# Optimization experiments

Hardware: AMD Instinct MI355X
Metric: run time of the kernel (lower is better)

Reference implementation:

```python
import jax, jax.numpy as jnp
import numpy as np

L_SEG = 20   # number of CFT segments (hard-coded in original forward)
M_CHEB = 8   # Chebyshev quadrature order per segment


def _cft_magnitude(x, modes):
    """|CFT(x)| at integer frequencies [0, modes).

    Faithful to vectorized_batched_cft_decomposed with L=20, M=8, but only
    evaluated at the first `modes` frequencies (identical values; the original
    computes all rfft freqs then slices). Segment loop is folded into a single
    einsum by absorbing the per-segment phase shift into the quadrature weights.
    x: (B, C, N) real. Returns (B, C, modes) float.
    """
    n = x.shape[-1]
    t = jnp.linspace(0.0, 1.0, n)
    freqs = jnp.arange(modes, dtype=x.dtype)  # rfftfreq(n, d=1/n)[:modes]
    seg_len = 1.0 / L_SEG
    starts = jnp.linspace(0.0, 1.0, L_SEG + 1)[:-1]  # (L,)
    k = jnp.arange(M_CHEB, dtype=x.dtype)
    cheb = -jnp.cos((2.0 * k + 1.0) * jnp.pi / (2.0 * M_CHEB))  # (M,) nodes in [-1,1]
    T = jnp.cos(k[:, None] * jnp.arccos(cheb)[None, :])  # (K=M, M) Chebyshev T_k at nodes
    angle = cheb[:, None] * (freqs[None, :] * (2.0 * jnp.pi * seg_len / 2.0))  # (M, F)
    Wr = jnp.einsum('km,mf->kf', T, jnp.cos(angle)) * (seg_len / 2.0)  # (M, F)
    Wi = jnp.einsum('km,mf->kf', T, -jnp.sin(angle)) * (seg_len / 2.0)
    # piecewise-linear interpolation of x at the Chebyshev nodes of every segment
    t_seg = starts[:, None] + seg_len / 2.0 * (cheb + 1.0)[None, :]  # (L, M)
    right = jnp.clip(jnp.searchsorted(t, t_seg), 0, n - 1)
    left = jnp.clip(right - 1, 0, None)
    t_l, t_r = t[left], t[right]
    denom = jnp.where(t_r - t_l == 0.0, 1.0, t_r - t_l)
    w_r = (t_seg - t_l) / denom
    w_l = 1.0 - w_r
    seg = w_l * x[:, :, left] + w_r * x[:, :, right]  # (B, C, L, M)
    # per-segment phase shift exp(-i*2*pi*f*a) folded into combined weights
    phi = 2.0 * jnp.pi * starts[:, None] * freqs[None, :]  # (L, F)
    cs, sn = jnp.cos(phi), jnp.sin(phi)
    Ar = Wr[None] * cs[:, None, :] + Wi[None] * sn[:, None, :]   # (L, M, F)
    Ai = -Wr[None] * sn[:, None, :] + Wi[None] * cs[:, None, :]
    real = jnp.einsum('bclm,lmf->bcf', seg, Ar)
    imag = jnp.einsum('bclm,lmf->bcf', seg, Ai)
    return jnp.sqrt(real * real + imag * imag)


def setup_inputs() -> dict:
    key = jax.random.key(0)
    ks = jax.random.split(key, 4)
    B, Cin, Cout, N, modes = 32, 64, 64, 8192, 32
    scale = 1.0 / (Cin * Cout)
    return {
        'x': jax.random.normal(ks[0], (B, Cin, N), dtype=jnp.float32),
        'w1_real': scale * jax.random.uniform(ks[1], (Cin, Cout, modes), dtype=jnp.float32),
        'w1_imag': scale * jax.random.uniform(ks[2], (Cin, Cout, modes), dtype=jnp.float32),
        'gate_w': jax.random.normal(ks[3], (Cout, Cin), dtype=jnp.float32) / np.sqrt(Cin),
        'ln_gamma': jnp.ones((modes,), dtype=jnp.float32),
        'ln_beta': jnp.zeros((modes,), dtype=jnp.float32),
    }


def reference(x, w1_real, w1_imag, gate_w, ln_gamma, ln_beta):
    n = x.shape[-1]
    n_rfft = n // 2 + 1
    modes = w1_real.shape[-1]
    x_fft = jnp.fft.rfft(x)  # (B, C, n_rfft) complex64
    # CFT magnitude is detached in the original (x_cft.detach())
    mag = jax.lax.stop_gradient(_cft_magnitude(x, modes))  # (B, C, modes)
    # LayerNorm over the modes axis (eps = 1e-5, torch default)
    mu = jnp.mean(mag, axis=-1, keepdims=True)
    var = jnp.mean((mag - mu) ** 2, axis=-1, keepdims=True)
    g_norm = (mag - mu) / jnp.sqrt(var + 1e-5) * ln_gamma + ln_beta
    # 1x1 conv (no bias) over channels, then sigmoid gate
    gate = jax.nn.sigmoid(jnp.einsum('oi,bif->bof', gate_w, g_norm))  # (B, Cout, modes)
    gated = x_fft[:, :, :modes] * gate  # requires Cin == Cout
    w1 = w1_real + 1j * w1_imag  # (Cin, Cout, modes) complex
    out_modes = jnp.einsum('bix,iox->box', gated, w1)
    pad = jnp.zeros(out_modes.shape[:2] + (n_rfft - modes,), dtype=out_modes.dtype)
    out_ft = jnp.concatenate([out_modes, pad], axis=-1)
    return jnp.fft.irfft(out_ft, n=n)
```

## Files before the change

### kernel.cpp

```cpp
#include <hip/hip_runtime.h>
#include <hip/hip_bf16.h>
#include <math.h>

#define NN    8192
#define NROWS 2048
#define FF    32
#define LM    160

static constexpr int TRIG   = 0;
static constexpr int W1RT   = 524288;
static constexpr int W1IT   = 655360;
static constexpr int GWT    = 786432;
static constexpr int AR_    = 790528;
static constexpr int AI_    = 795648;
static constexpr int WL_    = 800768;
static constexpr int WR_    = 800928;
static constexpr int IL_    = 801088;
static constexpr int IR_    = 801248;
static constexpr int XR_    = 801408;
static constexpr int XI_    = 866944;
static constexpr int GN_    = 932480;
static constexpr int ARAI   = 998016;
static constexpr int TRIGT_ = 1129088;

#define PI_D 3.14159265358979323846

__device__ __forceinline__ void load_lds16(const float* g, float* l) {
  __builtin_amdgcn_global_load_lds(
      (const __attribute__((address_space(1))) void*)g,
      (__attribute__((address_space(3))) void*)l, 16, 0, 0);
}

__global__ __launch_bounds__(256) void k_trig(float* __restrict__ ws) {
  int idx = blockIdx.x * 256 + threadIdx.x;
  int k4 = idx >> 8, f = (idx >> 2) & 63, j = idx & 3;
  int n = 4 * k4 + j;
  int fr = f & 31;
  int p = (fr * n) & (NN - 1);
  float ang = (float)p * (float)(2.0 * PI_D / (double)NN);
  float s, c;
  sincosf(ang, &s, &c);
  float v = (f < 32) ? c : s;
  ws[TRIG + idx] = v;
  ws[TRIGT_ + f * NN + n] = v;
}

__global__ __launch_bounds__(256) void k_cft_tables(float* __restrict__ ws) {
  int tid = blockIdx.x * 256 + threadIdx.x;
  if (tid >= LM * FF) return;
  int j = tid >> 5, f = tid & 31;
  int l = j >> 3, m = j & 7;
  const double cheb[8] = {
    -0.98078528040323044913, -0.83146961230254523708,
    -0.55557023301960222474, -0.19509032201612826785,
     0.19509032201612826785,  0.55557023301960222474,
     0.83146961230254523708,  0.98078528040323044913 };

  double Wr = 0.0, Wi = 0.0;
  #pragma unroll
  for (int mm = 0; mm < 8; ++mm) {
    double c = cheb[mm];
    double T;
    if (m == 0) T = 1.0;
    else {
      double a = 1.0, b = c;
      for (int q = 1; q < m; ++q) { double t = 2.0 * c * b - a; a = b; b = t; }
      T = b;
    }
    double ang = c * (double)f * (PI_D * 0.05);
    Wr += T * cos(ang);
    Wi += T * (-sin(ang));
  }
  Wr *= 0.025; Wi *= 0.025;
  double phi = 2.0 * PI_D * ((double)l * 0.05) * (double)f;
  double cs = cos(phi), sn = sin(phi);
  ws[AR_ + j * FF + f] = (float)(Wr * cs + Wi * sn);
  ws[AI_ + j * FF + f] = (float)(-Wr * sn + Wi * cs);

  if (f == 0) {
    double v = (double)l * 0.05 + 0.025 * (cheb[m] + 1.0);
    int r = (int)(v * 8191.0);
    while ((double)r / 8191.0 < v) ++r;
    while (r > 0 && (double)(r - 1) / 8191.0 >= v) --r;
    if (r > 8191) r = 8191;
    int le = r - 1; if (le < 0) le = 0;
    double tl = (double)le / 8191.0, tr = (double)r / 8191.0;
    double den = (tr - tl == 0.0) ? 1.0 : (tr - tl);
    double wr = (v - tl) / den;
    ws[WL_ + j] = (float)(1.0 - wr);
    ws[WR_ + j] = (float)wr;
    ((int*)ws)[IL_ + j] = le;
    ((int*)ws)[IR_ + j] = r;
  }
}

__global__ __launch_bounds__(256) void k_transpose(const float* __restrict__ w1r,
                                                   const float* __restrict__ w1i,
                                                   const float* __restrict__ gw,
                                                   float* __restrict__ ws) {
  int idx = blockIdx.x * 256 + threadIdx.x;
  if (idx >= 32 * 64 * 64) return;
  int o = idx & 63, i = (idx >> 6) & 63, f = idx >> 12;
  ws[W1RT + (f * 64 + i) * 64 + o] = w1r[(i * 64 + o) * FF + f];
  ws[W1IT + (f * 64 + i) * 64 + o] = w1i[(i * 64 + o) * FF + f];
  if (idx < 4096) {
    ws[GWT + idx] = gw[(idx & 63) * 64 + (idx >> 6)];
  }
}

__global__ __launch_bounds__(256) void k_fwd_gemm(const float* __restrict__ x,
                                                  const float* __restrict__ ws,
                                                  float* __restrict__ part) {
  __shared__ __align__(16) float xs[64 * 128];
  __shared__ __align__(16) float ts[32 * 256];
  const int rt = blockIdx.x >> 6, kc = blockIdx.x & 63;
  const int t = threadIdx.x;
  const int w = t >> 6, lane = t & 63;
  const int half = lane >> 5, fl = lane & 31;
  const int rblock = rt * 64;
  const int kb = kc * 128;
  const int c4 = t & 31, r0 = t >> 5;

  #pragma unroll
  for (int p = 0; p < 8; ++p) {
    int row = r0 + 8 * p;
    load_lds16(x + (size_t)(rblock + row) * NN + kb + c4 * 4,
               &xs[row * 128 + c4 * 4]);
  }
  const float* __restrict__ tsrc = ws + TRIG + (size_t)kc * 8192;
  #pragma unroll
  for (int p = 0; p < 8; ++p) {
    int q = 256 * p + t;
    load_lds16(tsrc + q * 4, &ts[q * 4]);
  }

  float accC[8], accS[8];
  #pragma unroll
  for (int r = 0; r < 8; ++r) { accC[r] = 0.f; accS[r] = 0.f; }

  __syncthreads();

  const float* __restrict__ xb = &xs[(w * 16 + half * 8) * 128];
  const float* __restrict__ tb = &ts[fl * 4];

  #pragma unroll 8
  for (int it = 0; it < 32; ++it) {
    float4 tc = *(const float4*)(tb + it * 256);
    float4 tn = *(const float4*)(tb + it * 256 + 128);
    #pragma unroll
    for (int j = 0; j < 8; ++j) {
      float4 xv = *(const float4*)(xb + j * 128 + it * 4);
      accC[j] = fmaf(xv.w, tc.w, fmaf(xv.z, tc.z,
                fmaf(xv.y, tc.y, fmaf(xv.x, tc.x, accC[j]))));
      accS[j] = fmaf(xv.w, tn.w, fmaf(xv.z, tn.z,
                fmaf(xv.y, tn.y, fmaf(xv.x, tn.x, accS[j]))));
    }
  }

  float* __restrict__ pp = part + ((size_t)kc * NROWS + rblock + w * 16 + half * 8) * 64;
  #pragma unroll
  for (int j = 0; j < 8; ++j) {
    pp[j * 64 + fl]      = accC[j];
    pp[j * 64 + 32 + fl] = accS[j];
  }
}

__global__ __launch_bounds__(256) void k_fred(const float* __restrict__ part,
                                              float* __restrict__ ws) {
  int idx = blockIdx.x * 256 + threadIdx.x;
  int row = idx >> 4, fq = idx & 15;
  const float4* __restrict__ p4 = (const float4*)part;
  float4 s = make_float4(0.f, 0.f, 0.f, 0.f);
  #pragma unroll 16
  for (int kc = 0; kc < 64; ++kc) {
    float4 v = p4[((size_t)kc * NROWS + row) * 16 + fq];
    s.x += v.x; s.y += v.y; s.z += v.z; s.w += v.w;
  }
  if (fq < 8) {
    *(float4*)(ws + XR_ + row * FF + fq * 4) = s;
  } else {
    float4 n = make_float4(-s.x, -s.y, -s.z, -s.w);
    *(float4*)(ws + XI_ + row * FF + (fq - 8) * 4) = n;
  }
}

__global__ __launch_bounds__(256) void k_cft(const float* __restrict__ x,
                                             const float* __restrict__ gamma,
                                             const float* __restrict__ beta,
                                             float* __restrict__ ws) {
  const int sub = threadIdx.x >> 6, li = threadIdx.x & 63;
  const int row = blockIdx.x * 4 + sub;
  const float* __restrict__ xr = x + (size_t)row * NN;
  __shared__ float seg[4][LM];
  #pragma unroll
  for (int g = 0; g < 3; ++g) {
    int j = li + 64 * g;
    if (j < LM) {
      int il = ((const int*)ws)[IL_ + j];
      int ir = ((const int*)ws)[IR_ + j];
      seg[sub][j] = ws[WL_ + j] * xr[il] + ws[WR_ + j] * xr[ir];
    }
  }
  __syncthreads();
  if (li < FF) {
    float re = 0.f, im = 0.f;
    #pragma unroll 8
    for (int j = 0; j < LM; ++j) {
      float sv = seg[sub][j];
      re = fmaf(sv, ws[AR_ + j * FF + li], re);
      im = fmaf(sv, ws[AI_ + j * FF + li], im);
    }
    float mag = sqrtf(re * re + im * im);
    float mu = mag;
    mu += __shfl_xor(mu, 1);  mu += __shfl_xor(mu, 2);  mu += __shfl_xor(mu, 4);
    mu += __shfl_xor(mu, 8);  mu += __shfl_xor(mu, 16);
    mu *= (1.0f / 32.0f);
    float d = mag - mu;
    float vv = d * d;
    vv += __shfl_xor(vv, 1);  vv += __shfl_xor(vv, 2);  vv += __shfl_xor(vv, 4);
    vv += __shfl_xor(vv, 8);  vv += __shfl_xor(vv, 16);
    vv *= (1.0f / 32.0f);
    float g = d / sqrtf(vv + 1e-5f) * gamma[li] + beta[li];
    ws[GN_ + row * FF + li] = g;
  }
}

__global__ __launch_bounds__(64) void k_gate(float* __restrict__ ws) {
  int bidx = blockIdx.x;
  int b = bidx >> 5, f = bidx & 31;
  int o = threadIdx.x;
  __shared__ float gn[64], gr[64], gi[64];
  int rowb = b * 64;
  gn[o] = ws[GN_ + (rowb + o) * FF + f];
  float xre = ws[XR_ + (rowb + o) * FF + f];
  float xim = ws[XI_ + (rowb + o) * FF + f];
  __syncthreads();
  float acc = 0.f;
  #pragma unroll 16
  for (int i = 0; i < 64; ++i)
    acc = fmaf(ws[GWT + i * 64 + o], gn[i], acc);
  float gate = 1.0f / (1.0f + expf(-acc));
  gr[o] = xre * gate;
  gi[o] = xim * gate;
  __syncthreads();
  float Yr = 0.f, Yi = 0.f;
  const float* __restrict__ w1rt = ws + W1RT + f * 4096;
  const float* __restrict__ w1it = ws + W1IT + f * 4096;
  #pragma unroll 8
  for (int i = 0; i < 64; ++i) {
    float a = gr[i], bb2 = gi[i];
    float wr = w1rt[i * 64 + o], wi = w1it[i * 64 + o];
    Yr = fmaf(a, wr, Yr); Yr = fmaf(-bb2, wi, Yr);
    Yi = fmaf(a, wi, Yi); Yi = fmaf(bb2, wr, Yi);
  }
  float* A = ws + ARAI + (size_t)(rowb + o) * 64;
  if (f == 0) {
    A[0]  = Yr * (1.0f / (float)NN);
    A[32] = 0.0f;
  } else {
    A[f]      = Yr * (2.0f / (float)NN);
    A[32 + f] = -Yi * (2.0f / (float)NN);
  }
}

__global__ __launch_bounds__(256) void k_inv(const float* __restrict__ ws,
                                             float* __restrict__ out) {
  __shared__ __align__(16) float As[32 * 64];
  const int blk = blockIdx.x;
  const int bb = blk >> 5, cc = blk & 31;
  const int t = threadIdx.x;
  const int w = t >> 6, lane = t & 63;
  const int rowbase = bb * 32;
  const float* __restrict__ trigt = ws + TRIGT_;
  const int colb = cc * 256 + lane * 4;

  float4 tg0 = *(const float4*)(trigt + (size_t)0 * NN + colb);
  float4 tg1 = *(const float4*)(trigt + (size_t)1 * NN + colb);
  float4 tg2 = *(const float4*)(trigt + (size_t)2 * NN + colb);
  float4 tg3 = *(const float4*)(trigt + (size_t)3 * NN + colb);

  #pragma unroll
  for (int p = 0; p < 2; ++p) {
    int idx = t + 256 * p;
    int r = idx >> 4, q = idx & 15;
    *(float4*)(&As[r * 64 + q * 4]) =
        *(const float4*)(ws + ARAI + (size_t)(rowbase + r) * 64 + q * 4);
  }

  float4 acc[8];
  #pragma unroll
  for (int r = 0; r < 8; ++r) acc[r] = make_float4(0.f, 0.f, 0.f, 0.f);

  __syncthreads();

#define INV_STEP(F0)                                                            \
  {                                                                             \
    _Pragma("unroll")                                                           \
    for (int r = 0; r < 8; ++r) {                                               \
      float4 av = *(const float4*)(&As[(w * 8 + r) * 64 + (F0)]);               \
      acc[r].x = fmaf(av.x, tg0.x, acc[r].x); acc[r].y = fmaf(av.x, tg0.y, acc[r].y); \
      acc[r].z = fmaf(av.x, tg0.z, acc[r].z); acc[r].w = fmaf(av.x, tg0.w, acc[r].w); \
      acc[r].x = fmaf(av.y, tg1.x, acc[r].x); acc[r].y = fmaf(av.y, tg1.y, acc[r].y); \
      acc[r].z = fmaf(av.y, tg1.z, acc[r].z); acc[r].w = fmaf(av.y, tg1.w, acc[r].w); \
      acc[r].x = fmaf(av.z, tg2.x, acc[r].x); acc[r].y = fmaf(av.z, tg2.y, acc[r].y); \
      acc[r].z = fmaf(av.z, tg2.z, acc[r].z); acc[r].w = fmaf(av.z, tg2.w, acc[r].w); \
      acc[r].x = fmaf(av.w, tg3.x, acc[r].x); acc[r].y = fmaf(av.w, tg3.y, acc[r].y); \
      acc[r].z = fmaf(av.w, tg3.z, acc[r].z); acc[r].w = fmaf(av.w, tg3.w, acc[r].w); \
    }                                                                           \
  }

  for (int fo = 0; fo < 15; ++fo) {
    int f0 = fo * 4;
    float4 n0 = *(const float4*)(trigt + (size_t)(f0 + 4) * NN + colb);
    float4 n1 = *(const float4*)(trigt + (size_t)(f0 + 5) * NN + colb);
    float4 n2 = *(const float4*)(trigt + (size_t)(f0 + 6) * NN + colb);
    float4 n3 = *(const float4*)(trigt + (size_t)(f0 + 7) * NN + colb);
    INV_STEP(f0);
    tg0 = n0; tg1 = n1; tg2 = n2; tg3 = n3;
  }
  INV_STEP(60);
#undef INV_STEP

  #pragma unroll
  for (int r = 0; r < 8; ++r) {
    int row = rowbase + w * 8 + r;
    *(float4*)(out + (size_t)row * NN + colb) = acc[r];
  }
}

extern "C" void kernel_launch(void* const* d_in, const int* in_sizes, int n_in,
                              void* d_out, int out_size, void* d_ws, size_t ws_size,
                              hipStream_t stream) {
  const float* x     = (const float*)d_in[0];
  const float* w1r   = (const float*)d_in[1];
  const float* w1i   = (const float*)d_in[2];
  const float* gw    = (const float*)d_in[3];
  const float* gamma = (const float*)d_in[4];
  const float* beta  = (const float*)d_in[5];
  float* out = (float*)d_out;
  float* ws = (float*)d_ws;
  float* part = (float*)d_out;

  hipLaunchKernelGGL(k_trig,       dim3(2048), dim3(256), 0, stream, ws);
  hipLaunchKernelGGL(k_cft_tables, dim3(20),   dim3(256), 0, stream, ws);
  hipLaunchKernelGGL(k_transpose,  dim3(512),  dim3(256), 0, stream, w1r, w1i, gw, ws);
  hipLaunchKernelGGL(k_fwd_gemm,   dim3(2048), dim3(256), 0, stream, x, ws, part);
  hipLaunchKernelGGL(k_fred,       dim3(128),  dim3(256), 0, stream, part, ws);
  hipLaunchKernelGGL(k_cft,        dim3(512),  dim3(256), 0, stream, x, gamma, beta, ws);
  hipLaunchKernelGGL(k_gate,       dim3(1024), dim3(64),  0, stream, ws);
  hipLaunchKernelGGL(k_inv,        dim3(2048), dim3(256), 0, stream, ws, out);
}
```

Before: 214.9 us.

## Exploit half-period symmetry to halve forward and inverse DFT trig work

The forward DFT now folds x[n] and x[n+N/2] into sum and difference terms, so even frequencies use the sum and odd frequencies use the difference. This halves the trig table and the reduction length per block. The inverse DFT splits accumulation into even- and odd-frequency parts over half the columns, then writes both halves as E+O and E-O. Grid sizes and the trig table size are halved. The cost is extra LDS for the u/v buffers and twice as many accumulator registers in the inverse kernel.

Result: faster. 179.9 us (-16.3%).

```diff
diff --git a/kernel.cpp b/kernel.cpp
--- a/kernel.cpp
+++ b/kernel.cpp
@@ -3,6 +3,7 @@
 #include <math.h>
 
 #define NN    8192
+#define NH    4096
 #define NROWS 2048
 #define FF    32
 #define LM    160
@@ -33,8 +34,8 @@
 
 __global__ __launch_bounds__(256) void k_trig(float* __restrict__ ws) {
   int idx = blockIdx.x * 256 + threadIdx.x;
-  int k4 = idx >> 8, f = (idx >> 2) & 63, j = idx & 3;
-  int n = 4 * k4 + j;
+  int k4 = idx >> 8, f = (idx >> 2) & 63, e = idx & 3;
+  int n = 4 * k4 + e;
   int fr = f & 31;
   int p = (fr * n) & (NN - 1);
   float ang = (float)p * (float)(2.0 * PI_D / (double)NN);
@@ -42,7 +43,7 @@
   sincosf(ang, &s, &c);
   float v = (f < 32) ? c : s;
   ws[TRIG + idx] = v;
-  ws[TRIGT_ + f * NN + n] = v;
+  ws[TRIGT_ + f * NH + n] = v;
 }
 
 __global__ __launch_bounds__(256) void k_cft_tables(float* __restrict__ ws) {
@@ -111,45 +112,51 @@
 __global__ __launch_bounds__(256) void k_fwd_gemm(const float* __restrict__ x,
                                                   const float* __restrict__ ws,
                                                   float* __restrict__ part) {
-  __shared__ __align__(16) float xs[64 * 128];
-  __shared__ __align__(16) float ts[32 * 256];
-  const int rt = blockIdx.x >> 6, kc = blockIdx.x & 63;
+  __shared__ __align__(16) float uw[4096 + 16 + 4096];
+  __shared__ __align__(16) float ts[16 * 256];
+  const int rt = blockIdx.x >> 6, jc = blockIdx.x & 63;
   const int t = threadIdx.x;
   const int w = t >> 6, lane = t & 63;
   const int half = lane >> 5, fl = lane & 31;
   const int rblock = rt * 64;
-  const int kb = kc * 128;
-  const int c4 = t & 31, r0 = t >> 5;
-
-  #pragma unroll
-  for (int p = 0; p < 8; ++p) {
-    int row = r0 + 8 * p;
-    load_lds16(x + (size_t)(rblock + row) * NN + kb + c4 * 4,
-               &xs[row * 128 + c4 * 4]);
-  }
-  const float* __restrict__ tsrc = ws + TRIG + (size_t)kc * 8192;
-  #pragma unroll
-  for (int p = 0; p < 8; ++p) {
+  const int jb = jc * 64;
+
+  const float* __restrict__ tsrc = ws + TRIG + (size_t)jc * 4096;
+  #pragma unroll
+  for (int p = 0; p < 4; ++p) {
     int q = 256 * p + t;
     load_lds16(tsrc + q * 4, &ts[q * 4]);
   }
 
+  #pragma unroll
+  for (int p = 0; p < 4; ++p) {
+    int idx = 256 * p + t;
+    int row = idx >> 4, c4 = idx & 15;
+    const float* __restrict__ xp = x + (size_t)(rblock + row) * NN + jb + c4 * 4;
+    float4 a = *(const float4*)xp;
+    float4 b = *(const float4*)(xp + NH);
+    float4 u = make_float4(a.x + b.x, a.y + b.y, a.z + b.z, a.w + b.w);
+    float4 v = make_float4(a.x - b.x, a.y - b.y, a.z - b.z, a.w - b.w);
+    *(float4*)(&uw[row * 64 + c4 * 4]) = u;
+    *(float4*)(&uw[4112 + row * 64 + c4 * 4]) = v;
+  }
+
   float accC[8], accS[8];
   #pragma unroll
   for (int r = 0; r < 8; ++r) { accC[r] = 0.f; accS[r] = 0.f; }
 
   __syncthreads();
 
-  const float* __restrict__ xb = &xs[(w * 16 + half * 8) * 128];
+  const float* __restrict__ xb = &uw[(fl & 1) * 4112 + (w * 16 + half * 8) * 64];
   const float* __restrict__ tb = &ts[fl * 4];
 
-  #pragma unroll 8
-  for (int it = 0; it < 32; ++it) {
+  #pragma unroll
+  for (int it = 0; it < 16; ++it) {
     float4 tc = *(const float4*)(tb + it * 256);
     float4 tn = *(const float4*)(tb + it * 256 + 128);
     #pragma unroll
     for (int j = 0; j < 8; ++j) {
-      float4 xv = *(const float4*)(xb + j * 128 + it * 4);
+      float4 xv = *(const float4*)(xb + j * 64 + it * 4);
       accC[j] = fmaf(xv.w, tc.w, fmaf(xv.z, tc.z,
                 fmaf(xv.y, tc.y, fmaf(xv.x, tc.x, accC[j]))));
       accS[j] = fmaf(xv.w, tn.w, fmaf(xv.z, tn.z,
@@ -157,7 +164,7 @@
     }
   }
 
-  float* __restrict__ pp = part + ((size_t)kc * NROWS + rblock + w * 16 + half * 8) * 64;
+  float* __restrict__ pp = part + ((size_t)jc * NROWS + rblock + w * 16 + half * 8) * 64;
   #pragma unroll
   for (int j = 0; j < 8; ++j) {
     pp[j * 64 + fl]      = accC[j];
@@ -267,17 +274,17 @@
                                              float* __restrict__ out) {
   __shared__ __align__(16) float As[32 * 64];
   const int blk = blockIdx.x;
-  const int bb = blk >> 5, cc = blk & 31;
+  const int bb = blk >> 4, cc = blk & 15;
   const int t = threadIdx.x;
   const int w = t >> 6, lane = t & 63;
   const int rowbase = bb * 32;
   const float* __restrict__ trigt = ws + TRIGT_;
   const int colb = cc * 256 + lane * 4;
 
-  float4 tg0 = *(const float4*)(trigt + (size_t)0 * NN + colb);
-  float4 tg1 = *(const float4*)(trigt + (size_t)1 * NN + colb);
-  float4 tg2 = *(const float4*)(trigt + (size_t)2 * NN + colb);
-  float4 tg3 = *(const float4*)(trigt + (size_t)3 * NN + colb);
+  float4 tg0 = *(const float4*)(trigt + (size_t)0 * NH + colb);
+  float4 tg1 = *(const float4*)(trigt + (size_t)1 * NH + colb);
+  float4 tg2 = *(const float4*)(trigt + (size_t)2 * NH + colb);
+  float4 tg3 = *(const float4*)(trigt + (size_t)3 * NH + colb);
 
   #pragma unroll
   for (int p = 0; p < 2; ++p) {
@@ -287,9 +294,12 @@
         *(const float4*)(ws + ARAI + (size_t)(rowbase + r) * 64 + q * 4);
   }
 
-  float4 acc[8];
-  #pragma unroll
-  for (int r = 0; r < 8; ++r) acc[r] = make_float4(0.f, 0.f, 0.f, 0.f);
+  float4 accE[8], accO[8];
+  #pragma unroll
+  for (int r = 0; r < 8; ++r) {
+    accE[r] = make_float4(0.f, 0.f, 0.f, 0.f);
+    accO[r] = make_float4(0.f, 0.f, 0.f, 0.f);
+  }
 
   __syncthreads();
 
@@ -298,23 +308,23 @@
     _Pragma("unroll")                                                           \
     for (int r = 0; r < 8; ++r) {                                               \
       float4 av = *(const float4*)(&As[(w * 8 + r) * 64 + (F0)]);               \
-      acc[r].x = fmaf(av.x, tg0.x, acc[r].x); acc[r].y = fmaf(av.x, tg0.y, acc[r].y); \
-      acc[r].z = fmaf(av.x, tg0.z, acc[r].z); acc[r].w = fmaf(av.x, tg0.w, acc[r].w); \
-      acc[r].x = fmaf(av.y, tg1.x, acc[r].x); acc[r].y = fmaf(av.y, tg1.y, acc[r].y); \
-      acc[r].z = fmaf(av.y, tg1.z, acc[r].z); acc[r].w = fmaf(av.y, tg1.w, acc[r].w); \
-      acc[r].x = fmaf(av.z, tg2.x, acc[r].x); acc[r].y = fmaf(av.z, tg2.y, acc[r].y); \
-      acc[r].z = fmaf(av.z, tg2.z, acc[r].z); acc[r].w = fmaf(av.z, tg2.w, acc[r].w); \
-      acc[r].x = fmaf(av.w, tg3.x, acc[r].x); acc[r].y = fmaf(av.w, tg3.y, acc[r].y); \
-      acc[r].z = fmaf(av.w, tg3.z, acc[r].z); acc[r].w = fmaf(av.w, tg3.w, acc[r].w); \
+      accE[r].x = fmaf(av.x, tg0.x, accE[r].x); accE[r].y = fmaf(av.x, tg0.y, accE[r].y); \
+      accE[r].z = fmaf(av.x, tg0.z, accE[r].z); accE[r].w = fmaf(av.x, tg0.w, accE[r].w); \
+      accO[r].x = fmaf(av.y, tg1.x, accO[r].x); accO[r].y = fmaf(av.y, tg1.y, accO[r].y); \
+      accO[r].z = fmaf(av.y, tg1.z, accO[r].z); accO[r].w = fmaf(av.y, tg1.w, accO[r].w); \
+      accE[r].x = fmaf(av.z, tg2.x, accE[r].x); accE[r].y = fmaf(av.z, tg2.y, accE[r].y); \
+      accE[r].z = fmaf(av.z, tg2.z, accE[r].z); accE[r].w = fmaf(av.z, tg2.w, accE[r].w); \
+      accO[r].x = fmaf(av.w, tg3.x, accO[r].x); accO[r].y = fmaf(av.w, tg3.y, accO[r].y); \
+      accO[r].z = fmaf(av.w, tg3.z, accO[r].z); accO[r].w = fmaf(av.w, tg3.w, accO[r].w); \
     }                                                                           \
   }
 
   for (int fo = 0; fo < 15; ++fo) {
     int f0 = fo * 4;
-    float4 n0 = *(const float4*)(trigt + (size_t)(f0 + 4) * NN + colb);
-    float4 n1 = *(const float4*)(trigt + (size_t)(f0 + 5) * NN + colb);
-    float4 n2 = *(const float4*)(trigt + (size_t)(f0 + 6) * NN + colb);
-    float4 n3 = *(const float4*)(trigt + (size_t)(f0 + 7) * NN + colb);
+    float4 n0 = *(const float4*)(trigt + (size_t)(f0 + 4) * NH + colb);
+    float4 n1 = *(const float4*)(trigt + (size_t)(f0 + 5) * NH + colb);
+    float4 n2 = *(const float4*)(trigt + (size_t)(f0 + 6) * NH + colb);
+    float4 n3 = *(const float4*)(trigt + (size_t)(f0 + 7) * NH + colb);
     INV_STEP(f0);
     tg0 = n0; tg1 = n1; tg2 = n2; tg3 = n3;
   }
@@ -324,7 +334,11 @@
   #pragma unroll
   for (int r = 0; r < 8; ++r) {
     int row = rowbase + w * 8 + r;
-    *(float4*)(out + (size_t)row * NN + colb) = acc[r];
+    float4 E = accE[r], O = accO[r];
+    float4 s0 = make_float4(E.x + O.x, E.y + O.y, E.z + O.z, E.w + O.w);
+    float4 s1 = make_float4(E.x - O.x, E.y - O.y, E.z - O.z, E.w - O.w);
+    *(float4*)(out + (size_t)row * NN + colb)      = s0;
+    *(float4*)(out + (size_t)row * NN + colb + NH) = s1;
   }
 }
 
@@ -341,12 +355,12 @@
   float* ws = (float*)d_ws;
   float* part = (float*)d_out;
 
-  hipLaunchKernelGGL(k_trig,       dim3(2048), dim3(256), 0, stream, ws);
+  hipLaunchKernelGGL(k_trig,       dim3(1024), dim3(256), 0, stream, ws);
   hipLaunchKernelGGL(k_cft_tables, dim3(20),   dim3(256), 0, stream, ws);
   hipLaunchKernelGGL(k_transpose,  dim3(512),  dim3(256), 0, stream, w1r, w1i, gw, ws);
   hipLaunchKernelGGL(k_fwd_gemm,   dim3(2048), dim3(256), 0, stream, x, ws, part);
   hipLaunchKernelGGL(k_fred,       dim3(128),  dim3(256), 0, stream, part, ws);
   hipLaunchKernelGGL(k_cft,        dim3(512),  dim3(256), 0, stream, x, gamma, beta, ws);
   hipLaunchKernelGGL(k_gate,       dim3(1024), dim3(64),  0, stream, ws);
-  hipLaunchKernelGGL(k_inv,        dim3(2048), dim3(256), 0, stream, ws, out);
-}
+  hipLaunchKernelGGL(k_inv,        dim3(1024), dim3(256), 0, stream, ws, out);
+}
```
